# Optimization experiments

Measured on AMD Instinct MI355X. Metric: run time of the kernel, lower is better.

## Reference

```python
import jax, jax.numpy as jnp
import numpy as np

N = 200000      # nodes
C = 256         # scalar channels
VC = 16         # vector channels
VD = 3          # vector spatial dim
M = 50000       # number of motifs (segments)


def setup_inputs() -> dict:
    key = jax.random.key(0)
    ks, kv, kb, kw1, kb1, kw2, kb2 = jax.random.split(key, 7)
    s = jax.random.normal(ks, (N, C), dtype=jnp.float32)
    v = jax.random.normal(kv, (N, VC, VD), dtype=jnp.float32)
    motif_batch = jax.random.randint(kb, (N,), 0, M, dtype=jnp.int64)
    # Linear(channels, channels)
    Ws = jax.random.normal(kw1, (C, C), dtype=jnp.float32) / np.sqrt(C)
    bs = jax.random.normal(kb1, (C,), dtype=jnp.float32) * 0.01
    # Linear(16, 16)
    Wv = jax.random.normal(kw2, (VC, VC), dtype=jnp.float32) / np.sqrt(VC)
    bv = jax.random.normal(kb2, (VC,), dtype=jnp.float32) * 0.01
    return {"s": s, "v": v, "motif_batch": motif_batch,
            "Ws": Ws, "bs": bs, "Wv": Wv, "bv": bv}


def _scatter_mean(x, seg, num_segments):
    # robust scatter mean: sum / max(count, 1)
    sums = jax.ops.segment_sum(x, seg, num_segments=num_segments)
    cnt = jax.ops.segment_sum(jnp.ones((x.shape[0],), x.dtype), seg,
                              num_segments=num_segments)
    cnt = jnp.maximum(cnt, 1.0)
    return sums / cnt.reshape((num_segments,) + (1,) * (x.ndim - 1))


def reference(s, v, motif_batch, Ws, bs, Wv, bv):
    seg = motif_batch.reshape(-1)
    s_motif = _scatter_mean(s, seg, M)            # [M, C]
    v_motif = _scatter_mean(v, seg, M)            # [M, VC, VD]
    s_out = s_motif @ Ws.T + bs                   # [M, C]
    # v_pool(v_motif.transpose(1,2)).transpose(1,2):
    # Linear over the VC axis, spatial dim untouched
    v_out = jnp.einsum('mcd,oc->mod', v_motif, Wv) + bv[None, :, None]
    return (s_out, v_out)
```

## Files before the change

kernel.cpp:

```cpp
#include <hip/hip_runtime.h>

#define N_NODES 200000
#define C 256
#define VC 16
#define VD 3
#define VDIM (VC * VD)
#define M_MOTIFS 50000
#define CAP 64

#define TM 16
#define NODE_BLOCKS ((N_NODES + 255) / 256)
#define CVT_BLOCKS  ((C * C) / (256 * 4))
#define FUSED_BLOCKS (M_MOTIFS / TM)

typedef __attribute__((ext_vector_type(8))) __bf16 bf16x8;
typedef __attribute__((ext_vector_type(4))) float f32x4;

__device__ __forceinline__ unsigned short f2bf(float x) {
  unsigned u = __builtin_bit_cast(unsigned, x);
  u += 0x7fffu + ((u >> 16) & 1u);
  return (unsigned short)(u >> 16);
}

__global__ __launch_bounds__(256) void fill_kernel(
    const int* __restrict__ seg, int* __restrict__ cnt,
    int* __restrict__ nodelist, const float* __restrict__ Ws,
    unsigned short* __restrict__ Wsb) {
  int b = blockIdx.x, t = threadIdx.x;
  if (b < NODE_BLOCKS) {
    int i = b * 256 + t;
    if (i < N_NODES) {
      int m = seg[i];
      int r = atomicAdd(&cnt[m], 1);
      if (r < CAP) nodelist[(size_t)m * CAP + r] = i;
    }
  } else {
    int i = ((b - NODE_BLOCKS) * 256 + t) * 4;
    float4 w = *(const float4*)(Ws + i);
    ushort4 o;
    o.x = f2bf(w.x); o.y = f2bf(w.y); o.z = f2bf(w.z); o.w = f2bf(w.w);
    *(ushort4*)(Wsb + i) = o;
  }
}

__global__ __launch_bounds__(256, 6) void fused_kernel(
    const float* __restrict__ s, const float* __restrict__ v,
    const int* __restrict__ cnt, const int* __restrict__ nodelist,
    const unsigned short* __restrict__ Wsb, const float* __restrict__ bs,
    const float* __restrict__ Wv, const float* __restrict__ bv,
    float* __restrict__ s_out, float* __restrict__ v_out) {
  __shared__ unsigned short As[TM * C];

  int tid = threadIdx.x;
  int wave = tid >> 6, lane = tid & 63;
  int bm0 = blockIdx.x * TM;
  int m0w = bm0 + wave * 4;

  int kvv = 0;
  if (lane < 4) kvv = cnt[m0w + lane];
  int mr = lane >> 4, sl = lane & 15;
  int idv = nodelist[(size_t)(m0w + mr) * CAP + sl];

  for (int r = 0; r < 4; ++r) {
    int m = m0w + r;
    int k = __shfl(kvv, r, 64);
    int kc = min(k, CAP);
    int n16 = min(kc, 16);
    int rb = r * 16;
    float4 acc = make_float4(0.f, 0.f, 0.f, 0.f);
    float vacc = 0.f;
    int jj = 0;
    for (; jj + 4 <= n16; jj += 4) {
      int i0 = __shfl(idv, rb + jj + 0, 64);
      int i1 = __shfl(idv, rb + jj + 1, 64);
      int i2 = __shfl(idv, rb + jj + 2, 64);
      int i3 = __shfl(idv, rb + jj + 3, 64);
      float4 a = ((const float4*)(s + (size_t)i0 * C))[lane];
      float4 b = ((const float4*)(s + (size_t)i1 * C))[lane];
      float4 c = ((const float4*)(s + (size_t)i2 * C))[lane];
      float4 d = ((const float4*)(s + (size_t)i3 * C))[lane];
      acc.x += (a.x + b.x) + (c.x + d.x);
      acc.y += (a.y + b.y) + (c.y + d.y);
      acc.z += (a.z + b.z) + (c.z + d.z);
      acc.w += (a.w + b.w) + (c.w + d.w);
      if (lane < VDIM) {
        float va = v[(size_t)i0 * VDIM + lane];
        float vb = v[(size_t)i1 * VDIM + lane];
        float vc = v[(size_t)i2 * VDIM + lane];
        float vd = v[(size_t)i3 * VDIM + lane];
        vacc += (va + vb) + (vc + vd);
      }
    }
    for (; jj < n16; ++jj) {
      int i0 = __shfl(idv, rb + jj, 64);
      float4 a = ((const float4*)(s + (size_t)i0 * C))[lane];
      acc.x += a.x; acc.y += a.y; acc.z += a.z; acc.w += a.w;
      if (lane < VDIM) vacc += v[(size_t)i0 * VDIM + lane];
    }
    for (int j = 16; j < kc; ++j) {
      int i0 = nodelist[(size_t)m * CAP + j];
      float4 a = ((const float4*)(s + (size_t)i0 * C))[lane];
      acc.x += a.x; acc.y += a.y; acc.z += a.z; acc.w += a.w;
      if (lane < VDIM) vacc += v[(size_t)i0 * VDIM + lane];
    }

    float rc = 1.0f / (float)max(k, 1);
    ushort4 o;
    o.x = f2bf(acc.x * rc); o.y = f2bf(acc.y * rc);
    o.z = f2bf(acc.z * rc); o.w = f2bf(acc.w * rc);
    int rblk = (wave << 2) + r;
    *(ushort4*)&As[rblk * C + ((lane * 4) ^ ((rblk & 7) << 3))] = o;

    float vm = vacc * rc;
    if (lane < VDIM) {
      int oo = lane / 3, d = lane - oo * 3;
      float vo = bv[oo];
#pragma unroll
      for (int c2 = 0; c2 < VC; ++c2)
        vo += Wv[oo * VC + c2] * __shfl(vm, c2 * 3 + d, 64);
      v_out[(size_t)m * VDIM + lane] = vo;
    }
  }

  __syncthreads();

  int rl = lane & 15, kq = (lane >> 4) * 8;
  int wn0 = wave * 64;
  int xorv = (rl & 7) << 3;
  f32x4 acc4[4] = {};
#pragma unroll
  for (int k0 = 0; k0 < C; k0 += 32) {
    bf16x8 af = *(const bf16x8*)&As[rl * C + ((k0 + kq) ^ xorv)];
    bf16x8 bfr[4];
#pragma unroll
    for (int j = 0; j < 4; ++j)
      bfr[j] = *(const bf16x8*)(Wsb + (size_t)(wn0 + j * 16 + rl) * C + k0 + kq);
#pragma unroll
    for (int j = 0; j < 4; ++j)
      acc4[j] = __builtin_amdgcn_mfma_f32_16x16x32_bf16(af, bfr[j], acc4[j],
                                                        0, 0, 0);
  }

  int rq = (lane >> 4) * 4;
#pragma unroll
  for (int j = 0; j < 4; ++j) {
    int cn = wn0 + j * 16 + rl;
    float bias = bs[cn];
#pragma unroll
    for (int rr = 0; rr < 4; ++rr) {
      int gm = bm0 + rq + rr;
      s_out[(size_t)gm * C + cn] = acc4[j][rr] + bias;
    }
  }
}

extern "C" void kernel_launch(void* const* d_in, const int* in_sizes, int n_in,
                              void* d_out, int out_size, void* d_ws, size_t ws_size,
                              hipStream_t stream) {
  const float* s  = (const float*)d_in[0];
  const float* v  = (const float*)d_in[1];
  const int*   seg = (const int*)d_in[2];
  const float* Ws = (const float*)d_in[3];
  const float* bs = (const float*)d_in[4];
  const float* Wv = (const float*)d_in[5];
  const float* bv = (const float*)d_in[6];

  float* out   = (float*)d_out;
  float* s_out = out;
  float* v_out = out + (size_t)M_MOTIFS * C;

  int* cnt      = (int*)d_ws;
  int* nodelist = cnt + M_MOTIFS;
  unsigned short* Wsb = (unsigned short*)(nodelist + (size_t)M_MOTIFS * CAP);

  hipMemsetAsync(cnt, 0, M_MOTIFS * sizeof(int), stream);
  fill_kernel<<<NODE_BLOCKS + CVT_BLOCKS, 256, 0, stream>>>(seg, cnt, nodelist,
                                                            Ws, Wsb);
  fused_kernel<<<FUSED_BLOCKS, 256, 0, stream>>>(s, v, cnt, nodelist, Wsb, bs,
                                                 Wv, bv, s_out, v_out);
}
```

Before: 120.7 us.

## Split fused gather+GEMM into separate gather kernel and tiled MFMA GEMM

```diff
diff --git a/kernel.cpp b/kernel.cpp
--- a/kernel.cpp
+++ b/kernel.cpp
@@ -6,12 +6,12 @@
 #define VD 3
 #define VDIM (VC * VD)
 #define M_MOTIFS 50000
+#define M_PAD 50048
 #define CAP 64
 
-#define TM 16
 #define NODE_BLOCKS ((N_NODES + 255) / 256)
 #define CVT_BLOCKS  ((C * C) / (256 * 4))
-#define FUSED_BLOCKS (M_MOTIFS / TM)
+#define GATHER_BLOCKS (M_MOTIFS / 4)
 
 typedef __attribute__((ext_vector_type(8))) __bf16 bf16x8;
 typedef __attribute__((ext_vector_type(4))) float f32x4;
@@ -20,6 +20,12 @@
   unsigned u = __builtin_bit_cast(unsigned, x);
   u += 0x7fffu + ((u >> 16) & 1u);
   return (unsigned short)(u >> 16);
+}
+
+__device__ __forceinline__ void async_copy16(const void* g, void* l) {
+  __builtin_amdgcn_global_load_lds(
+      (const __attribute__((address_space(1))) unsigned int*)g,
+      (__attribute__((address_space(3))) unsigned int*)l, 16, 0, 0);
 }
 
 __global__ __launch_bounds__(256) void fill_kernel(
@@ -43,113 +49,155 @@
   }
 }
 
-__global__ __launch_bounds__(256, 6) void fused_kernel(
+__global__ __launch_bounds__(256) void gather_kernel(
     const float* __restrict__ s, const float* __restrict__ v,
     const int* __restrict__ cnt, const int* __restrict__ nodelist,
-    const unsigned short* __restrict__ Wsb, const float* __restrict__ bs,
     const float* __restrict__ Wv, const float* __restrict__ bv,
-    float* __restrict__ s_out, float* __restrict__ v_out) {
-  __shared__ unsigned short As[TM * C];
-
+    unsigned short* __restrict__ s_motif, float* __restrict__ v_out) {
+  int m = (blockIdx.x * 256 + threadIdx.x) >> 6;
+  int lane = threadIdx.x & 63;
+  int k = cnt[m];
+
+  if (k == 0) {
+    ushort4 z; z.x = z.y = z.z = z.w = 0;
+    ((ushort4*)(s_motif + (size_t)m * C))[lane] = z;
+    if (lane < VDIM) v_out[(size_t)m * VDIM + lane] = bv[lane / 3];
+    return;
+  }
+
+  int idv = nodelist[(size_t)m * CAP + (lane & 15)];
+  int km1 = k - 1;
+  int kc = min(k, CAP);
+
+  int i0 = __shfl(idv, 0, 64);
+  int i1 = __shfl(idv, min(1, km1), 64);
+  int i2 = __shfl(idv, min(2, km1), 64);
+  int i3 = __shfl(idv, min(3, km1), 64);
+  float4 a0 = ((const float4*)(s + (size_t)i0 * C))[lane];
+  float4 a1 = ((const float4*)(s + (size_t)i1 * C))[lane];
+  float4 a2 = ((const float4*)(s + (size_t)i2 * C))[lane];
+  float4 a3 = ((const float4*)(s + (size_t)i3 * C))[lane];
+  float vb0 = 0.f, vb1 = 0.f, vb2 = 0.f, vb3 = 0.f;
+  if (lane < VDIM) {
+    vb0 = v[(size_t)i0 * VDIM + lane];
+    vb1 = v[(size_t)i1 * VDIM + lane];
+    vb2 = v[(size_t)i2 * VDIM + lane];
+    vb3 = v[(size_t)i3 * VDIM + lane];
+  }
+  float4 acc = a0;
+  float vacc = vb0;
+  if (k > 1) { acc.x += a1.x; acc.y += a1.y; acc.z += a1.z; acc.w += a1.w; vacc += vb1; }
+  if (k > 2) { acc.x += a2.x; acc.y += a2.y; acc.z += a2.z; acc.w += a2.w; vacc += vb2; }
+  if (k > 3) { acc.x += a3.x; acc.y += a3.y; acc.z += a3.z; acc.w += a3.w; vacc += vb3; }
+
+  if (k > 4) {
+    int i4 = __shfl(idv, min(4, km1), 64);
+    int i5 = __shfl(idv, min(5, km1), 64);
+    int i6 = __shfl(idv, min(6, km1), 64);
+    int i7 = __shfl(idv, min(7, km1), 64);
+    float4 b4 = ((const float4*)(s + (size_t)i4 * C))[lane];
+    float4 b5 = ((const float4*)(s + (size_t)i5 * C))[lane];
+    float4 b6 = ((const float4*)(s + (size_t)i6 * C))[lane];
+    float4 b7 = ((const float4*)(s + (size_t)i7 * C))[lane];
+    float w4 = 0.f, w5 = 0.f, w6 = 0.f, w7 = 0.f;
+    if (lane < VDIM) {
+      w4 = v[(size_t)i4 * VDIM + lane];
+      w5 = v[(size_t)i5 * VDIM + lane];
+      w6 = v[(size_t)i6 * VDIM + lane];
+      w7 = v[(size_t)i7 * VDIM + lane];
+    }
+    acc.x += b4.x; acc.y += b4.y; acc.z += b4.z; acc.w += b4.w; vacc += w4;
+    if (k > 5) { acc.x += b5.x; acc.y += b5.y; acc.z += b5.z; acc.w += b5.w; vacc += w5; }
+    if (k > 6) { acc.x += b6.x; acc.y += b6.y; acc.z += b6.z; acc.w += b6.w; vacc += w6; }
+    if (k > 7) { acc.x += b7.x; acc.y += b7.y; acc.z += b7.z; acc.w += b7.w; vacc += w7; }
+  }
+
+  if (k > 8) {
+    int idv2 = nodelist[(size_t)m * CAP + lane];
+    for (int j = 8; j < kc; ++j) {
+      int ij = __shfl(idv2, j, 64);
+      float4 a = ((const float4*)(s + (size_t)ij * C))[lane];
+      acc.x += a.x; acc.y += a.y; acc.z += a.z; acc.w += a.w;
+      if (lane < VDIM) vacc += v[(size_t)ij * VDIM + lane];
+    }
+  }
+
+  float rc = 1.0f / (float)k;
+  ushort4 o;
+  o.x = f2bf(acc.x * rc); o.y = f2bf(acc.y * rc);
+  o.z = f2bf(acc.z * rc); o.w = f2bf(acc.w * rc);
+  ((ushort4*)(s_motif + (size_t)m * C))[lane] = o;
+
+  float vm = vacc * rc;
+  if (lane < VDIM) {
+    int oo = lane / 3, d = lane - oo * 3;
+    float vo = bv[oo];
+#pragma unroll
+    for (int c2 = 0; c2 < VC; ++c2)
+      vo += Wv[oo * VC + c2] * __shfl(vm, c2 * 3 + d, 64);
+    v_out[(size_t)m * VDIM + lane] = vo;
+  }
+}
+
+__global__ __launch_bounds__(256) void gemm_mfma_kernel(
+    const unsigned short* __restrict__ A16,
+    const unsigned short* __restrict__ B16,
+    const float* __restrict__ bs, float* __restrict__ out) {
+  __shared__ unsigned short As[128 * 32];
+  __shared__ unsigned short Bs[128 * 32];
   int tid = threadIdx.x;
   int wave = tid >> 6, lane = tid & 63;
-  int bm0 = blockIdx.x * TM;
-  int m0w = bm0 + wave * 4;
-
-  int kvv = 0;
-  if (lane < 4) kvv = cnt[m0w + lane];
-  int mr = lane >> 4, sl = lane & 15;
-  int idv = nodelist[(size_t)(m0w + mr) * CAP + sl];
-
-  for (int r = 0; r < 4; ++r) {
-    int m = m0w + r;
-    int k = __shfl(kvv, r, 64);
-    int kc = min(k, CAP);
-    int n16 = min(kc, 16);
-    int rb = r * 16;
-    float4 acc = make_float4(0.f, 0.f, 0.f, 0.f);
-    float vacc = 0.f;
-    int jj = 0;
-    for (; jj + 4 <= n16; jj += 4) {
-      int i0 = __shfl(idv, rb + jj + 0, 64);
-      int i1 = __shfl(idv, rb + jj + 1, 64);
-      int i2 = __shfl(idv, rb + jj + 2, 64);
-      int i3 = __shfl(idv, rb + jj + 3, 64);
-      float4 a = ((const float4*)(s + (size_t)i0 * C))[lane];
-      float4 b = ((const float4*)(s + (size_t)i1 * C))[lane];
-      float4 c = ((const float4*)(s + (size_t)i2 * C))[lane];
-      float4 d = ((const float4*)(s + (size_t)i3 * C))[lane];
-      acc.x += (a.x + b.x) + (c.x + d.x);
-      acc.y += (a.y + b.y) + (c.y + d.y);
-      acc.z += (a.z + b.z) + (c.z + d.z);
-      acc.w += (a.w + b.w) + (c.w + d.w);
-      if (lane < VDIM) {
-        float va = v[(size_t)i0 * VDIM + lane];
-        float vb = v[(size_t)i1 * VDIM + lane];
-        float vc = v[(size_t)i2 * VDIM + lane];
-        float vd = v[(size_t)i3 * VDIM + lane];
-        vacc += (va + vb) + (vc + vd);
+  int m0 = blockIdx.x * 128;
+  int n0 = blockIdx.y * 128;
+  int wm = (wave >> 1) * 64, wn = (wave & 1) * 64;
+
+  f32x4 acc[4][4] = {};
+
+  int srow = lane >> 2;
+  int kc   = (lane & 3) * 8;
+  int rl = lane & 15;
+  int kq = (lane >> 4) * 8;
+
+  const unsigned short* Ag = A16 + (size_t)(m0 + wave * 32) * C;
+  const unsigned short* Bg = B16 + (size_t)(n0 + wave * 32) * C;
+  unsigned short* Al = As + wave * 32 * 32;
+  unsigned short* Bl = Bs + wave * 32 * 32;
+
+  for (int k0 = 0; k0 < C; k0 += 32) {
+    async_copy16(Ag + (size_t)srow * C + k0 + kc, Al);
+    async_copy16(Ag + (size_t)(16 + srow) * C + k0 + kc, Al + 16 * 32);
+    async_copy16(Bg + (size_t)srow * C + k0 + kc, Bl);
+    async_copy16(Bg + (size_t)(16 + srow) * C + k0 + kc, Bl + 16 * 32);
+    __syncthreads();
+
+    bf16x8 af[4], bfr[4];
+#pragma unroll
+    for (int i = 0; i < 4; ++i)
+      af[i] = *(const bf16x8*)&As[(size_t)(wm + i * 16 + rl) * 32 + kq];
+#pragma unroll
+    for (int j = 0; j < 4; ++j)
+      bfr[j] = *(const bf16x8*)&Bs[(size_t)(wn + j * 16 + rl) * 32 + kq];
+#pragma unroll
+    for (int i = 0; i < 4; ++i)
+#pragma unroll
+      for (int j = 0; j < 4; ++j)
+        acc[i][j] = __builtin_amdgcn_mfma_f32_16x16x32_bf16(
+            af[i], bfr[j], acc[i][j], 0, 0, 0);
+    __syncthreads();
+  }
+
+  int rq = (lane >> 4) * 4;
+#pragma unroll
+  for (int j = 0; j < 4; ++j) {
+    int cn = n0 + wn + j * 16 + rl;
+    float bias = bs[cn];
+#pragma unroll
+    for (int i = 0; i < 4; ++i) {
+#pragma unroll
+      for (int r = 0; r < 4; ++r) {
+        int gm = m0 + wm + i * 16 + rq + r;
+        if (gm < M_MOTIFS) out[(size_t)gm * C + cn] = acc[i][j][r] + bias;
       }
-    }
-    for (; jj < n16; ++jj) {
-      int i0 = __shfl(idv, rb + jj, 64);
-      float4 a = ((const float4*)(s + (size_t)i0 * C))[lane];
-      acc.x += a.x; acc.y += a.y; acc.z += a.z; acc.w += a.w;
-      if (lane < VDIM) vacc += v[(size_t)i0 * VDIM + lane];
-    }
-    for (int j = 16; j < kc; ++j) {
-      int i0 = nodelist[(size_t)m * CAP + j];
-      float4 a = ((const float4*)(s + (size_t)i0 * C))[lane];
-      acc.x += a.x; acc.y += a.y; acc.z += a.z; acc.w += a.w;
-      if (lane < VDIM) vacc += v[(size_t)i0 * VDIM + lane];
-    }
-
-    float rc = 1.0f / (float)max(k, 1);
-    ushort4 o;
-    o.x = f2bf(acc.x * rc); o.y = f2bf(acc.y * rc);
-    o.z = f2bf(acc.z * rc); o.w = f2bf(acc.w * rc);
-    int rblk = (wave << 2) + r;
-    *(ushort4*)&As[rblk * C + ((lane * 4) ^ ((rblk & 7) << 3))] = o;
-
-    float vm = vacc * rc;
-    if (lane < VDIM) {
-      int oo = lane / 3, d = lane - oo * 3;
-      float vo = bv[oo];
-#pragma unroll
-      for (int c2 = 0; c2 < VC; ++c2)
-        vo += Wv[oo * VC + c2] * __shfl(vm, c2 * 3 + d, 64);
-      v_out[(size_t)m * VDIM + lane] = vo;
-    }
-  }
-
-  __syncthreads();
-
-  int rl = lane & 15, kq = (lane >> 4) * 8;
-  int wn0 = wave * 64;
-  int xorv = (rl & 7) << 3;
-  f32x4 acc4[4] = {};
-#pragma unroll
-  for (int k0 = 0; k0 < C; k0 += 32) {
-    bf16x8 af = *(const bf16x8*)&As[rl * C + ((k0 + kq) ^ xorv)];
-    bf16x8 bfr[4];
-#pragma unroll
-    for (int j = 0; j < 4; ++j)
-      bfr[j] = *(const bf16x8*)(Wsb + (size_t)(wn0 + j * 16 + rl) * C + k0 + kq);
-#pragma unroll
-    for (int j = 0; j < 4; ++j)
-      acc4[j] = __builtin_amdgcn_mfma_f32_16x16x32_bf16(af, bfr[j], acc4[j],
-                                                        0, 0, 0);
-  }
-
-  int rq = (lane >> 4) * 4;
-#pragma unroll
-  for (int j = 0; j < 4; ++j) {
-    int cn = wn0 + j * 16 + rl;
-    float bias = bs[cn];
-#pragma unroll
-    for (int rr = 0; rr < 4; ++rr) {
-      int gm = bm0 + rq + rr;
-      s_out[(size_t)gm * C + cn] = acc4[j][rr] + bias;
     }
   }
 }
@@ -171,11 +219,16 @@
 
   int* cnt      = (int*)d_ws;
   int* nodelist = cnt + M_MOTIFS;
-  unsigned short* Wsb = (unsigned short*)(nodelist + (size_t)M_MOTIFS * CAP);
+  unsigned short* Wsb     = (unsigned short*)(nodelist + (size_t)M_MOTIFS * CAP);
+  unsigned short* s_motif = Wsb + (size_t)C * C;
 
   hipMemsetAsync(cnt, 0, M_MOTIFS * sizeof(int), stream);
   fill_kernel<<<NODE_BLOCKS + CVT_BLOCKS, 256, 0, stream>>>(seg, cnt, nodelist,
                                                             Ws, Wsb);
-  fused_kernel<<<FUSED_BLOCKS, 256, 0, stream>>>(s, v, cnt, nodelist, Wsb, bs,
-                                                 Wv, bv, s_out, v_out);
-}
+  gather_kernel<<<GATHER_BLOCKS, 256, 0, stream>>>(s, v, cnt, nodelist, Wv, bv,
+                                                   s_motif, v_out);
+  {
+    dim3 grid(M_PAD / 128, C / 128);
+    gemm_mfma_kernel<<<grid, 256, 0, stream>>>(s_motif, Wsb, bs, s_out);
+  }
+}
```

New measurement: 104.1 us. 13.8% less time.
